# Optimization experiments

Hardware: AMD Instinct MI355X
Metric: run time of the kernel (lower is better)

The kernel has to match this reference:

```python
import jax, jax.numpy as jnp
import numpy as np

B, F, H, W = 1, 6, 20, 26
S = F * H * W            # 3120 tokens
DIM, NH, HD = 1536, 12, 128
C = HD // 2              # 64 rotary channels
T_C = C - 2 * (C // 3)   # 22 temporal channels
H_C = C // 3             # 21
W_C = C // 3             # 21
LOCAL_FRAMES = 4         # local_attn_size (in frames)
SINK_FRAMES = 1          # sink_size (in frames)
EPS = 1e-6
MAX_POS = 1024


def _angle_table(n_ch):
    inv = 1.0 / (10000.0 ** (np.arange(n_ch, dtype=np.float64) / n_ch))
    return np.outer(np.arange(MAX_POS, dtype=np.float64), inv)


def setup_inputs() -> dict:
    key = jax.random.key(0)
    ks = jax.random.split(key, 8)
    sc = 0.02
    ang = np.concatenate([_angle_table(T_C), _angle_table(H_C), _angle_table(W_C)], axis=1)  # [1024, 64]
    return {
        "x": jax.random.normal(ks[0], (B, S, DIM), jnp.float32),
        "seq_lens": jnp.array([S], jnp.int32),
        "grid_sizes": jnp.array([[F, H, W]], jnp.int32),
        "freqs_cos": jnp.asarray(np.cos(ang), jnp.float32),
        "freqs_sin": jnp.asarray(np.sin(ang), jnp.float32),
        "Wq": jax.random.normal(ks[1], (DIM, DIM), jnp.float32) * sc,
        "bq": jnp.zeros((DIM,), jnp.float32),
        "Wk": jax.random.normal(ks[2], (DIM, DIM), jnp.float32) * sc,
        "bk": jnp.zeros((DIM,), jnp.float32),
        "Wv": jax.random.normal(ks[3], (DIM, DIM), jnp.float32) * sc,
        "bv": jnp.zeros((DIM,), jnp.float32),
        "Wo": jax.random.normal(ks[4], (DIM, DIM), jnp.float32) * sc,
        "bo": jnp.zeros((DIM,), jnp.float32),
        "gq": jnp.ones((DIM,), jnp.float32),
        "gk": jnp.ones((DIM,), jnp.float32),
    }


def _rms_norm(x, g):
    # WanRMSNorm: x * rsqrt(mean(x^2) + eps) * weight
    return x * jax.lax.rsqrt(jnp.mean(x * x, axis=-1, keepdims=True) + EPS) * g


def _rope_apply(x, freqs_cos, freqs_sin):
    # x: [B, S, NH, HD]; per-token 3D (f,h,w) rotary on consecutive pairs.
    pos = jnp.arange(S)
    f = pos // (H * W)
    hh = (pos // W) % H
    ww = pos % W
    cos_t, cos_h, cos_w = freqs_cos[:, :T_C], freqs_cos[:, T_C:T_C + H_C], freqs_cos[:, T_C + H_C:]
    sin_t, sin_h, sin_w = freqs_sin[:, :T_C], freqs_sin[:, T_C:T_C + H_C], freqs_sin[:, T_C + H_C:]
    cos = jnp.concatenate([cos_t[f], cos_h[hh], cos_w[ww]], axis=-1)[None, :, None, :]  # [1,S,1,C]
    sin = jnp.concatenate([sin_t[f], sin_h[hh], sin_w[ww]], axis=-1)[None, :, None, :]
    xp = x.reshape(B, S, NH, C, 2)
    xr, xi = xp[..., 0], xp[..., 1]
    out = jnp.stack([xr * cos - xi * sin, xr * sin + xi * cos], axis=-1)
    return out.reshape(B, S, NH, HD)


def _block_mask():
    # frame-causal + local window (in frames) + sink frames: [S, S] bool
    fid = jnp.arange(S) // (H * W)
    fi, fj = fid[:, None], fid[None, :]
    return (fj <= fi) & ((fi - fj < LOCAL_FRAMES) | (fj < SINK_FRAMES))


def reference(x, seq_lens, grid_sizes, freqs_cos, freqs_sin,
              Wq, bq, Wk, bk, Wv, bv, Wo, bo, gq, gk):
    q = _rms_norm(x @ Wq + bq, gq).reshape(B, S, NH, HD)
    k = _rms_norm(x @ Wk + bk, gk).reshape(B, S, NH, HD)
    v = (x @ Wv + bv).reshape(B, S, NH, HD)
    rq = _rope_apply(q, freqs_cos, freqs_sin)
    rk = _rope_apply(k, freqs_cos, freqs_sin)
    scale = 1.0 / jnp.sqrt(jnp.asarray(HD, x.dtype))
    scores = jnp.einsum('bind,bjnd->bnij', rq, rk) * scale  # [B,NH,S,S]
    scores = jnp.where(_block_mask()[None, None], scores, jnp.finfo(scores.dtype).min)
    attn = jax.nn.softmax(scores, axis=-1)
    out = jnp.einsum('bnij,bjnd->bind', attn, v).reshape(B, S, DIM)
    return out @ Wo + bo
```

## Files before the change

kernel.cpp:

```cpp
#include <hip/hip_runtime.h>
#include <hip/hip_bf16.h>
#include <stdint.h>

typedef short v8s __attribute__((ext_vector_type(8)));
typedef float v4f __attribute__((ext_vector_type(4)));
typedef unsigned short u16;

#define S_LEN 3120
#define DIMN 1536
#define NHEAD 12
#define HDIM 128
#define FRM 520
#define NT64 49
#define T64_PH 166
#define TOT64 1992
#define NSTEP32 17
#define SCALE_QK 0.088388347648318447f
#define MAXOFF 12.0f

struct TaskMap {
  unsigned char tile[T64_PH];
  unsigned char frame[T64_PH];
  short accv[NT64];
  unsigned char nf[NT64];
};
constexpr TaskMap make_map() {
  TaskMap m{};
  int acc = 0;
  for (int tile = 0; tile < NT64; ++tile) {
    int q0t = tile * 64;
    int f_lo = q0t / FRM;
    int qhi = q0t + 63 < S_LEN - 1 ? q0t + 63 : S_LEN - 1;
    int f_hi = qhi / FRM;
    int fstart = f_lo - 3 > 0 ? f_lo - 3 : 0;
    int sink = fstart > 0 ? 1 : 0;
    int nf = f_hi - fstart + 1 + sink;
    m.accv[tile] = (short)acc;
    m.nf[tile] = (unsigned char)nf;
    for (int c = 0; c < nf; ++c) {
      m.tile[acc + c] = (unsigned char)tile;
      m.frame[acc + c] = (unsigned char)(sink ? (c == 0 ? 0 : fstart + c - 1) : (fstart + c));
    }
    acc += nf;
  }
  return m;
}
__device__ __constant__ TaskMap TM = make_map();

__device__ __forceinline__ v4f mfma16(v8s a, v8s b, v4f c) {
  return __builtin_amdgcn_mfma_f32_16x16x32_bf16(a, b, c, 0, 0, 0);
}
__device__ __forceinline__ float b2f(u16 u) {
  union { float f; unsigned int i; } x; x.i = ((unsigned int)u) << 16; return x.f;
}
__device__ __forceinline__ u16 f2b(float f) {
  union { float f; unsigned int i; } x; x.f = f;
  unsigned int r = x.i + 0x7FFFu + ((x.i >> 16) & 1u);
  return (u16)(r >> 16);
}
__device__ __forceinline__ void async16(const void* g, void* l) {
  __builtin_amdgcn_global_load_lds(
      (__attribute__((address_space(1))) const void*)g,
      (__attribute__((address_space(3))) void*)l, 16, 0, 0);
}

__global__ void detect_dtype(const u16* __restrict__ w, int* __restrict__ flag) {
  __shared__ int sh;
  int t = threadIdx.x;
  if (t == 0) sh = 0;
  __syncthreads();
  u16 m0 = (u16)(w[2 * t] & 0x7FFF);
  u16 m1 = (u16)(w[2 * t + 1] & 0x7FFF);
  if (m0 >= 0x4480 || m1 >= 0x4480) atomicOr(&sh, 1);
  __syncthreads();
  if (t == 0) *flag = sh;
}

struct PrepArgs {
  const void* tin[4]; u16* tout[4];
  const void* csrc[9]; u16* cdst[9]; int cn[9];
};
__global__ __launch_bounds__(256) void prep(PrepArgs a, const int* __restrict__ flag) {
  int isf = *flag;
  int z = blockIdx.z;
  int t = threadIdx.x;
  if (z < 4) {
    __shared__ u16 tile[32][33];
    const float* inf = (const float*)a.tin[z];
    const u16* inb = (const u16*)a.tin[z];
    u16* out = a.tout[z];
    int tx = t & 31, ty = t >> 5;
    int gr0 = blockIdx.y * 32, gc0 = blockIdx.x * 32;
#pragma unroll
    for (int i = 0; i < 4; ++i) {
      int r = ty + i * 8;
      size_t idx = (size_t)(gr0 + r) * DIMN + gc0 + tx;
      tile[r][tx] = isf ? f2b(inf[idx]) : inb[idx];
    }
    __syncthreads();
#pragma unroll
    for (int i = 0; i < 4; ++i) {
      int r = ty + i * 8;
      out[(size_t)(gc0 + r) * DIMN + gr0 + tx] = tile[tx][r];
    }
  } else {
    int id = z - 4;
    int n = a.cn[id];
    const float* sf = (const float*)a.csrc[id];
    const u16* sb = (const u16*)a.csrc[id];
    u16* d = a.cdst[id];
    int bidx = blockIdx.y * gridDim.x + blockIdx.x;
    int stride = gridDim.x * gridDim.y * 256;
    for (int i = bidx * 256 + t; i < n; i += stride)
      d[i] = isf ? f2b(sf[i]) : sb[i];
  }
}

__global__ __launch_bounds__(256) void transpose16(const u16* __restrict__ in,
                                                   u16* __restrict__ out,
                                                   int rows, int cols) {
  __shared__ u16 tile[32][33];
  int t = threadIdx.x;
  int tx = t & 31, ty = t >> 5;
  int gr0 = blockIdx.y * 32, gc0 = blockIdx.x * 32;
#pragma unroll
  for (int i = 0; i < 4; ++i) {
    int r = ty + i * 8;
    int gr = gr0 + r, gc = gc0 + tx;
    if (gr < rows && gc < cols) tile[r][tx] = in[(size_t)gr * cols + gc];
  }
  __syncthreads();
#pragma unroll
  for (int i = 0; i < 4; ++i) {
    int r = ty + i * 8;
    int orow = gc0 + r, ocol = gr0 + tx;
    if (orow < cols && ocol < rows) out[(size_t)orow * rows + ocol] = tile[tx][r];
  }
}

template <int MT>
__global__ __launch_bounds__(256) void gemm3(
    const u16* __restrict__ A,
    const u16* BT0, const u16* BT1, const u16* BT2,
    const u16* b0, const u16* b1, const u16* b2,
    void* C0, void* C1, void* C2, int M, const int* __restrict__ flag, int dyn) {
  const u16* BT; const u16* bias; void* C;
  if (blockIdx.z == 0)      { BT = BT0; bias = b0; C = C0; }
  else if (blockIdx.z == 1) { BT = BT1; bias = b1; C = C1; }
  else                      { BT = BT2; bias = b2; C = C2; }
  int f32out = dyn ? *flag : 0;
  __shared__ __align__(16) short As[MT * 64];
  __shared__ __align__(16) short Bs[128 * 64];
  int t = threadIdx.x, w = t >> 6, l = t & 63;
  int ln = l & 15, lg = l >> 4;
  int m0 = blockIdx.y * MT, n0 = blockIdx.x * 128;
  int lr = l >> 3;
  int gl = (l & 7) ^ lr;
  constexpr int ACH = MT / 32;
  const u16* gAp[ACH]; short* lAp[ACH];
#pragma unroll
  for (int i = 0; i < ACH; ++i) {
    int c = w * ACH + i;
    int arow = min(m0 + c * 8 + lr, M - 1);
    gAp[i] = A + (size_t)arow * DIMN + gl * 8;
    lAp[i] = As + c * 512;
  }
  const u16* gBp[4]; short* lBp[4];
#pragma unroll
  for (int i = 0; i < 4; ++i) {
    int c = w * 4 + i;
    int brow = n0 + c * 8 + lr;
    gBp[i] = BT + (size_t)brow * DIMN + gl * 8;
    lBp[i] = Bs + c * 512;
  }
  constexpr int NJ = (MT == 128) ? 4 : 2;
  int wm = (MT == 128) ? (w & 1) : 0;
  int wn = (MT == 128) ? (w >> 1) : w;
  int aoff[2][4], boff[2][NJ];
#pragma unroll
  for (int ks = 0; ks < 2; ++ks) {
#pragma unroll
    for (int i = 0; i < 4; ++i) {
      int ar = wm * 64 + i * 16 + ln;
      aoff[ks][i] = ar * 64 + (((ks * 4 + lg) ^ (ar & 7)) * 8);
    }
#pragma unroll
    for (int j = 0; j < NJ; ++j) {
      int br = wn * (NJ * 16) + j * 16 + ln;
      boff[ks][j] = br * 64 + (((ks * 4 + lg) ^ (br & 7)) * 8);
    }
  }
  v4f acc[4][NJ] = {};
  for (int k0 = 0; k0 < DIMN; k0 += 64) {
    __syncthreads();
#pragma unroll
    for (int i = 0; i < ACH; ++i) async16(gAp[i] + k0, lAp[i]);
#pragma unroll
    for (int i = 0; i < 4; ++i) async16(gBp[i] + k0, lBp[i]);
    __syncthreads();
#pragma unroll
    for (int ks = 0; ks < 2; ++ks) {
      v8s af[4], bfr[NJ];
#pragma unroll
      for (int i = 0; i < 4; ++i) af[i] = *(const v8s*)(As + aoff[ks][i]);
#pragma unroll
      for (int j = 0; j < NJ; ++j) bfr[j] = *(const v8s*)(Bs + boff[ks][j]);
#pragma unroll
      for (int i = 0; i < 4; ++i)
#pragma unroll
        for (int j = 0; j < NJ; ++j) acc[i][j] = mfma16(af[i], bfr[j], acc[i][j]);
    }
  }
#pragma unroll
  for (int i = 0; i < 4; ++i) {
    int rb = m0 + wm * 64 + i * 16 + lg * 4;
#pragma unroll
    for (int j = 0; j < NJ; ++j) {
      int col = n0 + wn * (NJ * 16) + j * 16 + ln;
      float bv = b2f(bias[col]);
#pragma unroll
      for (int r = 0; r < 4; ++r) {
        int grow = rb + r;
        if (grow < M) {
          size_t idx = (size_t)grow * DIMN + col;
          float val = acc[i][j][r] + bv;
          if (f32out) ((float*)C)[idx] = val;
          else        ((u16*)C)[idx] = f2b(val);
        }
      }
    }
  }
}

__global__ __launch_bounds__(256) void norm_rope(u16* __restrict__ Q, u16* __restrict__ K,
                                                 const u16* __restrict__ gq,
                                                 const u16* __restrict__ gk,
                                                 const u16* __restrict__ fcos,
                                                 const u16* __restrict__ fsin) {
  int s = blockIdx.x;
  u16* base = (blockIdx.y == 0 ? Q : K) + (size_t)s * DIMN;
  const u16* g = (blockIdx.y == 0) ? gq : gk;
  int t = threadIdx.x;
  int e = t * 6;
  float x[6];
#pragma unroll
  for (int i = 0; i < 6; ++i) x[i] = b2f(base[e + i]);
  float ss = 0.f;
#pragma unroll
  for (int i = 0; i < 6; ++i) ss += x[i] * x[i];
#pragma unroll
  for (int off = 32; off > 0; off >>= 1) ss += __shfl_xor(ss, off);
  __shared__ float red[4];
  if ((t & 63) == 0) red[t >> 6] = ss;
  __syncthreads();
  float tot = red[0] + red[1] + red[2] + red[3];
  float rs = rsqrtf(tot * (1.0f / DIMN) + 1e-6f);
  int f = s / FRM;
  int hh = (s / 26) % 20;
  int ww = s % 26;
#pragma unroll
  for (int u = 0; u < 3; ++u) {
    int e0 = e + 2 * u;
    int c = (e0 & 127) >> 1;
    int p = (c < 22) ? f : ((c < 43) ? hh : ww);
    float co = b2f(fcos[p * 64 + c]);
    float si = b2f(fsin[p * 64 + c]);
    float xr = x[2 * u] * rs * b2f(g[e0]);
    float xi = x[2 * u + 1] * rs * b2f(g[e0 + 1]);
    base[e0]     = f2b(xr * co - xi * si);
    base[e0 + 1] = f2b(xr * si + xi * co);
  }
}

__global__ __launch_bounds__(128) void attn_block(const u16* __restrict__ Q,
                                                  const u16* __restrict__ K,
                                                  const u16* __restrict__ VT,
                                                  u16* __restrict__ Po,
                                                  float* __restrict__ Pl) {
  __shared__ __align__(16) short Ks[2][32 * 128];
  __shared__ __align__(16) short Vs[2][128 * 32];
  __shared__ __align__(16) short Pt[2][32 * 40];
  int t = threadIdx.x, w = t >> 6, l = t & 63;
  int ln = l & 15, lg = l >> 4;
  int task = blockIdx.x;
  int head = task / T64_PH, tid = task % T64_PH;
  int tile = TM.tile[tid], frame = TM.frame[tid];
  int q0 = tile * 64 + w * 32;
  v8s qf[2][4];
  bool rowok[2][4];
#pragma unroll
  for (int g = 0; g < 2; ++g) {
    int row = min(q0 + g * 16 + ln, S_LEN - 1);
    const u16* qp = Q + (size_t)row * DIMN + head * HDIM + lg * 8;
#pragma unroll
    for (int c = 0; c < 4; ++c) qf[g][c] = *(const v8s*)(qp + c * 32);
#pragma unroll
    for (int r = 0; r < 4; ++r) {
      int qr = q0 + g * 16 + lg * 4 + r;
      int fi = (qr < S_LEN) ? qr / FRM : -1;
      rowok[g][r] = (frame <= fi) && ((fi - frame) < 4 || frame == 0);
    }
  }
  float lsum[2][4] = {};
  v4f o[2][8] = {};
  int kbeg = frame * FRM, kend = kbeg + FRM;
  int kr_i[4], kgl_i[4], vd_i[4], vgl_i[4];
#pragma unroll
  for (int i = 0; i < 4; ++i) {
    int n = (w * 4 + i) * 64 + l;
    kr_i[i] = n >> 4;
    kgl_i[i] = (n & 15) ^ (kr_i[i] & 15);
    vd_i[i] = n >> 2;
    vgl_i[i] = (n & 3) ^ (vd_i[i] & 3);
  }
  const u16* Kb = K + head * HDIM;
  {
    int kb = kbeg;
#pragma unroll
    for (int i = 0; i < 4; ++i) {
      int krow = min(kb + kr_i[i], S_LEN - 1);
      async16(Kb + (size_t)krow * DIMN + kgl_i[i] * 8,
              (char*)Ks + (size_t)(w * 4 + i) * 1024);
      async16(VT + (size_t)(head * HDIM + vd_i[i]) * S_LEN + kb + vgl_i[i] * 8,
              (char*)Vs + (size_t)(w * 4 + i) * 1024);
    }
  }
  __syncthreads();
  for (int it = 0; it < NSTEP32; ++it) {
    int cur = it & 1;
    if (it + 1 < NSTEP32) {
      int kbn = kbeg + (it + 1) * 32;
      size_t boff = (size_t)(cur ^ 1) * 8192;
#pragma unroll
      for (int i = 0; i < 4; ++i) {
        int krow = min(kbn + kr_i[i], S_LEN - 1);
        async16(Kb + (size_t)krow * DIMN + kgl_i[i] * 8,
                (char*)Ks + boff + (size_t)(w * 4 + i) * 1024);
        async16(VT + (size_t)(head * HDIM + vd_i[i]) * S_LEN + kbn + vgl_i[i] * 8,
                (char*)Vs + boff + (size_t)(w * 4 + i) * 1024);
      }
    }
    int kb = kbeg + it * 32;
    v4f s[2][2] = {};
    __builtin_amdgcn_s_setprio(1);
#pragma unroll
    for (int kg = 0; kg < 2; ++kg) {
#pragma unroll
      for (int c = 0; c < 4; ++c) {
        v8s kf = *(const v8s*)(&Ks[cur][(kg * 16 + ln) * 128 + (((c * 4 + lg) ^ ln) * 8)]);
        s[0][kg] = mfma16(qf[0][c], kf, s[0][kg]);
        s[1][kg] = mfma16(qf[1][c], kf, s[1][kg]);
      }
    }
    __builtin_amdgcn_s_setprio(0);
#pragma unroll
    for (int g = 0; g < 2; ++g)
#pragma unroll
      for (int kg = 0; kg < 2; ++kg) {
        bool jv = (kb + kg * 16 + ln) < kend;
#pragma unroll
        for (int r = 0; r < 4; ++r) {
          float p = (rowok[g][r] && jv) ? __expf(s[g][kg][r] * SCALE_QK - MAXOFF) : 0.f;
          unsigned int bi = __float_as_uint(p) & 0xffff0000u;
          lsum[g][r] += __uint_as_float(bi);
          Pt[w][(g * 16 + lg * 4 + r) * 40 + kg * 16 + ln] = (u16)(bi >> 16);
        }
      }
    v8s pf0 = *(const v8s*)(&Pt[w][ln * 40 + lg * 8]);
    v8s pf1 = *(const v8s*)(&Pt[w][(16 + ln) * 40 + lg * 8]);
    __builtin_amdgcn_s_setprio(1);
#pragma unroll
    for (int d = 0; d < 8; ++d) {
      int rr = d * 16 + ln;
      v8s vf = *(const v8s*)(&Vs[cur][rr * 32 + ((lg ^ (rr & 3)) * 8)]);
      o[0][d] = mfma16(pf0, vf, o[0][d]);
      o[1][d] = mfma16(pf1, vf, o[1][d]);
    }
    __builtin_amdgcn_s_setprio(0);
    __syncthreads();
  }
#pragma unroll
  for (int g = 0; g < 2; ++g)
#pragma unroll
    for (int r = 0; r < 4; ++r) {
      float v = lsum[g][r];
      v += __shfl_xor(v, 1);
      v += __shfl_xor(v, 2);
      v += __shfl_xor(v, 4);
      v += __shfl_xor(v, 8);
      lsum[g][r] = v;
    }
  size_t pbase = (size_t)task * (64 * 128);
#pragma unroll
  for (int g = 0; g < 2; ++g)
#pragma unroll
    for (int d = 0; d < 8; ++d)
#pragma unroll
      for (int r = 0; r < 4; ++r) {
        int lrow = w * 32 + g * 16 + lg * 4 + r;
        Po[pbase + lrow * 128 + d * 16 + ln] = f2b(o[g][d][r]);
      }
  if (ln == 0) {
#pragma unroll
    for (int g = 0; g < 2; ++g)
#pragma unroll
      for (int r = 0; r < 4; ++r)
        Pl[task * 64 + w * 32 + g * 16 + lg * 4 + r] = lsum[g][r];
  }
}

__global__ __launch_bounds__(256) void attn_combine(const u16* __restrict__ Po,
                                                    const float* __restrict__ Pl,
                                                    u16* __restrict__ Oa) {
  int tile = blockIdx.x, h = blockIdx.y;
  int accv = TM.accv[tile], nf = TM.nf[tile];
  int base = h * T64_PH + accv;
  int t = threadIdx.x;
  int row = t >> 2, seg = (t & 3) * 32;
  int grow = tile * 64 + row;
  if (grow >= S_LEN) return;
  float lsum = 0.f;
  float ao[32];
#pragma unroll
  for (int j = 0; j < 32; ++j) ao[j] = 0.f;
  for (int c = 0; c < nf; ++c) {
    int task = base + c;
    lsum += Pl[task * 64 + row];
    const u16* p = Po + (size_t)task * 8192 + row * 128 + seg;
#pragma unroll
    for (int v = 0; v < 4; ++v) {
      v8s x = *(const v8s*)(p + v * 8);
#pragma unroll
      for (int j = 0; j < 8; ++j) ao[v * 8 + j] += b2f((u16)x[j]);
    }
  }
  float inv = 1.0f / lsum;
  u16* dst = Oa + (size_t)grow * DIMN + h * HDIM + seg;
#pragma unroll
  for (int v = 0; v < 4; ++v) {
    v8s res;
#pragma unroll
    for (int j = 0; j < 8; ++j) res[j] = (short)f2b(ao[v * 8 + j] * inv);
    *(v8s*)(dst + v * 8) = res;
  }
}

extern "C" void kernel_launch(void* const* d_in, const int* in_sizes, int n_in,
                              void* d_out, int out_size, void* d_ws, size_t ws_size,
                              hipStream_t stream) {
  (void)n_in; (void)out_size; (void)ws_size;
  int* flag = (int*)d_ws;
  u16* ws = (u16*)d_ws;
  size_t off = 16;
  const size_t SD = (size_t)S_LEN * DIMN;
  const size_t WW = (size_t)DIMN * DIMN;
  const size_t NPO = (size_t)1032 * 128 * 128;
  auto alloc = [&](size_t n) { u16* p = ws + off; off += (n + 7) & ~(size_t)7; return p; };
  u16* Xc  = alloc(SD);
  u16* Fc  = alloc(65536);
  u16* Fs  = alloc(65536);
  u16* bqc = alloc(1536); u16* bkc = alloc(1536); u16* bvc = alloc(1536); u16* boc = alloc(1536);
  u16* gqc = alloc(1536); u16* gkc = alloc(1536);
  u16* Qr = alloc(SD); u16* Kr = alloc(SD); u16* Vr = alloc(SD); u16* Oa = alloc(SD);
  u16* WoT = alloc(WW);
  u16* WqT = alloc(WW); u16* WkT = alloc(WW); u16* WvT = alloc(WW);
  alloc(NPO - 3 * WW);
  float* Pl = (float*)alloc((size_t)TOT64 * 64 * 2);
  u16* Po = WqT;
  u16* VT = Xc;

  detect_dtype<<<1, 256, 0, stream>>>((const u16*)d_in[5], flag);

  PrepArgs pa;
  pa.tin[0] = d_in[5];  pa.tout[0] = WqT;
  pa.tin[1] = d_in[7];  pa.tout[1] = WkT;
  pa.tin[2] = d_in[9];  pa.tout[2] = WvT;
  pa.tin[3] = d_in[11]; pa.tout[3] = WoT;
  const int srcIdx[9] = {0, 3, 4, 6, 8, 10, 12, 13, 14};
  u16* dsts[9] = {Xc, Fc, Fs, bqc, bkc, bvc, boc, gqc, gkc};
  for (int i = 0; i < 9; ++i) {
    pa.csrc[i] = d_in[srcIdx[i]];
    pa.cdst[i] = dsts[i];
    pa.cn[i] = in_sizes[srcIdx[i]];
  }
  dim3 b256(256);
  prep<<<dim3(48, 48, 13), b256, 0, stream>>>(pa, flag);
  gemm3<64><<<dim3(12, 49, 3), b256, 0, stream>>>(Xc, WqT, WkT, WvT, bqc, bkc, bvc,
                                                  Qr, Kr, Vr, S_LEN, flag, 0);
  norm_rope<<<dim3(S_LEN, 2), b256, 0, stream>>>(Qr, Kr, gqc, gkc, Fc, Fs);
  transpose16<<<dim3(48, 98), b256, 0, stream>>>(Vr, VT, S_LEN, DIMN);
  attn_block<<<dim3(TOT64), dim3(128), 0, stream>>>(Qr, Kr, VT, Po, Pl);
  attn_combine<<<dim3(NT64, NHEAD), b256, 0, stream>>>(Po, Pl, Oa);
  gemm3<64><<<dim3(12, 49, 1), b256, 0, stream>>>(Oa, WoT, WoT, WoT, boc, boc, boc,
                                                  d_out, d_out, d_out, S_LEN, flag, 1);
}
```

Measured before the change: 369.7 us.

## Load K and V fragments directly from global memory instead of LDS staging

```diff
diff --git a/kernel.cpp b/kernel.cpp
--- a/kernel.cpp
+++ b/kernel.cpp
@@ -277,8 +277,6 @@
                                                   const u16* __restrict__ VT,
                                                   u16* __restrict__ Po,
                                                   float* __restrict__ Pl) {
-  __shared__ __align__(16) short Ks[2][32 * 128];
-  __shared__ __align__(16) short Vs[2][128 * 32];
   __shared__ __align__(16) short Pt[2][32 * 40];
   int t = threadIdx.x, w = t >> 6, l = t & 63;
   int ln = l & 15, lg = l >> 4;
@@ -304,50 +302,25 @@
   float lsum[2][4] = {};
   v4f o[2][8] = {};
   int kbeg = frame * FRM, kend = kbeg + FRM;
-  int kr_i[4], kgl_i[4], vd_i[4], vgl_i[4];
-#pragma unroll
-  for (int i = 0; i < 4; ++i) {
-    int n = (w * 4 + i) * 64 + l;
-    kr_i[i] = n >> 4;
-    kgl_i[i] = (n & 15) ^ (kr_i[i] & 15);
-    vd_i[i] = n >> 2;
-    vgl_i[i] = (n & 3) ^ (vd_i[i] & 3);
-  }
-  const u16* Kb = K + head * HDIM;
-  {
-    int kb = kbeg;
-#pragma unroll
-    for (int i = 0; i < 4; ++i) {
-      int krow = min(kb + kr_i[i], S_LEN - 1);
-      async16(Kb + (size_t)krow * DIMN + kgl_i[i] * 8,
-              (char*)Ks + (size_t)(w * 4 + i) * 1024);
-      async16(VT + (size_t)(head * HDIM + vd_i[i]) * S_LEN + kb + vgl_i[i] * 8,
-              (char*)Vs + (size_t)(w * 4 + i) * 1024);
-    }
-  }
-  __syncthreads();
+  const u16* Kp = K + (size_t)head * HDIM + lg * 8;
+  const u16* Vp[8];
+#pragma unroll
+  for (int d = 0; d < 8; ++d)
+    Vp[d] = VT + (size_t)(head * HDIM + d * 16 + ln) * S_LEN + lg * 8;
   for (int it = 0; it < NSTEP32; ++it) {
-    int cur = it & 1;
-    if (it + 1 < NSTEP32) {
-      int kbn = kbeg + (it + 1) * 32;
-      size_t boff = (size_t)(cur ^ 1) * 8192;
-#pragma unroll
-      for (int i = 0; i < 4; ++i) {
-        int krow = min(kbn + kr_i[i], S_LEN - 1);
-        async16(Kb + (size_t)krow * DIMN + kgl_i[i] * 8,
-                (char*)Ks + boff + (size_t)(w * 4 + i) * 1024);
-        async16(VT + (size_t)(head * HDIM + vd_i[i]) * S_LEN + kbn + vgl_i[i] * 8,
-                (char*)Vs + boff + (size_t)(w * 4 + i) * 1024);
-      }
-    }
     int kb = kbeg + it * 32;
+    v8s vf[8];
+#pragma unroll
+    for (int d = 0; d < 8; ++d) vf[d] = *(const v8s*)(Vp[d] + kb);
     v4f s[2][2] = {};
     __builtin_amdgcn_s_setprio(1);
 #pragma unroll
     for (int kg = 0; kg < 2; ++kg) {
+      int krow = min(kb + kg * 16 + ln, S_LEN - 1);
+      const u16* kp = Kp + (size_t)krow * DIMN;
 #pragma unroll
       for (int c = 0; c < 4; ++c) {
-        v8s kf = *(const v8s*)(&Ks[cur][(kg * 16 + ln) * 128 + (((c * 4 + lg) ^ ln) * 8)]);
+        v8s kf = *(const v8s*)(kp + c * 32);
         s[0][kg] = mfma16(qf[0][c], kf, s[0][kg]);
         s[1][kg] = mfma16(qf[1][c], kf, s[1][kg]);
       }
@@ -371,13 +344,10 @@
     __builtin_amdgcn_s_setprio(1);
 #pragma unroll
     for (int d = 0; d < 8; ++d) {
-      int rr = d * 16 + ln;
-      v8s vf = *(const v8s*)(&Vs[cur][rr * 32 + ((lg ^ (rr & 3)) * 8)]);
-      o[0][d] = mfma16(pf0, vf, o[0][d]);
-      o[1][d] = mfma16(pf1, vf, o[1][d]);
+      o[0][d] = mfma16(pf0, vf[d], o[0][d]);
+      o[1][d] = mfma16(pf1, vf[d], o[1][d]);
     }
     __builtin_amdgcn_s_setprio(0);
-    __syncthreads();
   }
 #pragma unroll
   for (int g = 0; g < 2; ++g)
```

Result: slower. 410.0 us (+10.9%).
